# Optimization experiments

Hardware: AMD Instinct MI355X
Metric: run time of the kernel (lower is better)

## Reference

```python
import jax, jax.numpy as jnp
import numpy as np

B, H, L, D = 1, 8, 2048, 64
DP = 3   # positional coord dim
RE = 1   # extra relative features appended via concat
F = DP + RE  # LazyLinear in-features


def setup_inputs() -> dict:
    key = jax.random.key(0)
    ks = jax.random.split(key, 12)
    return {
        "q": jax.random.normal(ks[0], (B, H, L, D), jnp.float32),
        "k": jax.random.normal(ks[1], (B, H, L, D), jnp.float32),
        "v": jax.random.normal(ks[2], (B, H, L, D), jnp.float32),
        "c": jax.random.uniform(ks[3], (B, 1, 1, L), jnp.float32),
        "d_q": jax.random.normal(ks[4], (B, L, DP), jnp.float32),
        "d_k_top": jax.random.normal(ks[5], (B, L, DP), jnp.float32),
        "d_k_bot": jax.random.normal(ks[6], (B, L, DP), jnp.float32),
        "d_k_score": jax.random.uniform(ks[7], (B, L, 2, F), jnp.float32),
        "relative_top": jax.random.normal(ks[8], (B, L, L, RE), jnp.float32),
        "relative_bottom": jax.random.normal(ks[9], (B, L, L, RE), jnp.float32),
        "W_w": jax.random.normal(ks[10], (F, H), jnp.float32) * 0.1,
        "W_b": jax.random.normal(ks[11], (F, H), jnp.float32) * 0.1,
    }


def _pairwise_diff(a, b):
    # a: [B,Lq,Dp], b: [B,Lk,Dp] -> [B,Lq,Lk,Dp]
    return a[:, :, None, :] - b[:, None, :, :]


def reference(q, k, v, c, d_q, d_k_top, d_k_bot, d_k_score,
              relative_top, relative_bottom, W_w, W_b):
    # score function: scaled dot product -> [B,H,Lq,Lk]
    scores = jnp.einsum('bhqd,bhkd->bhqk', q, k) * (q.shape[-1] ** -0.5)

    # relative-position bias path
    dt = jnp.concatenate([_pairwise_diff(d_q, d_k_top), relative_top], axis=-1)     # [B,Lq,Lk,F]
    db = jnp.concatenate([_pairwise_diff(d_q, d_k_bot), relative_bottom], axis=-1)  # [B,Lq,Lk,F]
    dm = jnp.stack([dt, db], axis=3)                 # [B,Lq,Lk,2,F]
    dm = dm * d_k_score[:, None]                     # broadcast over Lq
    dm = dm.sum(axis=3)                              # [B,Lq,Lk,F]

    w = jax.nn.softplus(dm @ W_w).transpose(0, 3, 1, 2)  # [B,H,Lq,Lk]
    b = (dm @ W_b).transpose(0, 3, 1, 2)                 # [B,H,Lq,Lk]
    scores = scores * w + b

    # leaky probability function: softmax gated by per-key sampling weights c
    probs = jax.nn.softmax(scores, axis=-1) * c      # [B,H,Lq,Lk]

    out = jnp.einsum('bhqk,bhkd->bhqd', probs, v)
    return out, probs
```

## Files before the change

### kernel.cpp

```cpp
#include <hip/hip_runtime.h>
#include <cstdint>
#include <cstddef>

#define NH 8
#define LQ 2048
#define DH 64
#define NKT_Q 8

typedef __attribute__((ext_vector_type(8))) __bf16 bf16x8;
typedef __attribute__((ext_vector_type(8))) unsigned short ushort8;
typedef __attribute__((ext_vector_type(4))) float floatx4;

__device__ __forceinline__ unsigned short bf_trunc(float x) {
    return (unsigned short)(__float_as_uint(x) >> 16);
}
__device__ __forceinline__ float bf_up(unsigned short h) {
    return __uint_as_float(((unsigned int)h) << 16);
}
__device__ __forceinline__ unsigned short bf_rne(float x) {
    unsigned int u = __float_as_uint(x);
    return (unsigned short)((u + 0x7FFFu + ((u >> 16) & 1u)) >> 16);
}
struct hl_t { unsigned short h, l; };
__device__ __forceinline__ hl_t split2(float x) {
    hl_t r;
    r.h = bf_trunc(x);
    r.l = bf_trunc(x - bf_up(r.h));
    return r;
}

#define MFMA16(A, B, C) __builtin_amdgcn_mfma_f32_16x16x32_bf16((A), (B), (C), 0, 0, 0)

template <bool FAST>
__global__ __launch_bounds__(256, 3) void attn_main(
    const float* __restrict__ qp,  const float* __restrict__ kp,
    const float* __restrict__ vp,  const float* __restrict__ cp,
    const float* __restrict__ dqp, const float* __restrict__ dktp,
    const float* __restrict__ dkbp,const float* __restrict__ dksp,
    const float* __restrict__ rtp, const float* __restrict__ rbp,
    const float* __restrict__ Wwp, const float* __restrict__ Wbp,
    float* __restrict__ probp, float* __restrict__ lws, float* __restrict__ pvws,
    unsigned short* __restrict__ ews)
{
    __shared__ unsigned short sh_khi[64 * 72];
    __shared__ unsigned short sh_klo[64 * 72];
    __shared__ unsigned short sh_vhi[64 * 72];
    __shared__ unsigned short sh_vlo[64 * 72];
    __shared__ float sh_meta[64 * 13];
    __shared__ float sh_dqs[64 * 3];

    const int bid  = blockIdx.x;
    const int quar = bid & 3;
    const int h    = (bid >> 2) & 7;
    const int qt   = bid >> 5;
    const int q0   = qt * 64;
    const int t    = threadIdx.x;
    const int lane = t & 63;
    const int m    = lane & 15;
    const int quad = lane >> 4;
    const int w16  = (t >> 6) * 16;

    float Ww[4], Wb[4];
#pragma unroll
    for (int f = 0; f < 4; ++f) { Ww[f] = Wwp[f * NH + h]; Wb[f] = Wbp[f * NH + h]; }

    {
        const int row = t >> 2, s = t & 3;
        const float* src = qp + ((size_t)(h * LQ + q0 + row)) * DH + s * 16;
        ushort8 vh0, vh1, vl0, vl1;
#pragma unroll
        for (int j = 0; j < 2; ++j) {
            float4 x = *(const float4*)(src + 4 * j);
            hl_t a = split2(x.x * 0.125f), b = split2(x.y * 0.125f);
            hl_t c = split2(x.z * 0.125f), d = split2(x.w * 0.125f);
            vh0[4 * j + 0] = a.h; vl0[4 * j + 0] = a.l;
            vh0[4 * j + 1] = b.h; vl0[4 * j + 1] = b.l;
            vh0[4 * j + 2] = c.h; vl0[4 * j + 2] = c.l;
            vh0[4 * j + 3] = d.h; vl0[4 * j + 3] = d.l;
        }
#pragma unroll
        for (int j = 0; j < 2; ++j) {
            float4 x = *(const float4*)(src + 8 + 4 * j);
            hl_t a = split2(x.x * 0.125f), b = split2(x.y * 0.125f);
            hl_t c = split2(x.z * 0.125f), d = split2(x.w * 0.125f);
            vh1[4 * j + 0] = a.h; vl1[4 * j + 0] = a.l;
            vh1[4 * j + 1] = b.h; vl1[4 * j + 1] = b.l;
            vh1[4 * j + 2] = c.h; vl1[4 * j + 2] = c.l;
            vh1[4 * j + 3] = d.h; vl1[4 * j + 3] = d.l;
        }
        const int base = row * 72 + s * 16;
        *(ushort8*)&sh_khi[base] = vh0;  *(ushort8*)&sh_khi[base + 8] = vh1;
        *(ushort8*)&sh_klo[base] = vl0;  *(ushort8*)&sh_klo[base + 8] = vl1;
        if (t < 64) {
            sh_dqs[t * 3 + 0] = dqp[(q0 + t) * 3 + 0];
            sh_dqs[t * 3 + 1] = dqp[(q0 + t) * 3 + 1];
            sh_dqs[t * 3 + 2] = dqp[(q0 + t) * 3 + 2];
        }
    }
    __syncthreads();

    bf16x8 aqh[2], aql[2];
#pragma unroll
    for (int kc = 0; kc < 2; ++kc) {
        aqh[kc] = *(const bf16x8*)&sh_khi[(w16 + m) * 72 + kc * 32 + quad * 8];
        aql[kc] = *(const bf16x8*)&sh_klo[(w16 + m) * 72 + kc * 32 + quad * 8];
    }
    float dq0[4], dq1[4], dq2[4];
#pragma unroll
    for (int r = 0; r < 4; ++r) {
        const int row = w16 + quad * 4 + r;
        dq0[r] = sh_dqs[row * 3 + 0]; dq1[r] = sh_dqs[row * 3 + 1]; dq2[r] = sh_dqs[row * 3 + 2];
    }
    __syncthreads();

    const floatx4 zf = {0.f, 0.f, 0.f, 0.f};
    floatx4 pacc[4] = {zf, zf, zf, zf};
    float lpart[4] = {0.f, 0.f, 0.f, 0.f};

    for (int kth = 0; kth < NKT_Q; ++kth) {
        const int k0 = (quar * NKT_Q + kth) * 64;

        {
            const int row = t >> 2, s = t & 3;
            const float* src = kp + ((size_t)(h * LQ + k0 + row)) * DH + s * 16;
            ushort8 vh0, vh1, vl0, vl1;
#pragma unroll
            for (int j = 0; j < 2; ++j) {
                float4 x = *(const float4*)(src + 4 * j);
                hl_t a = split2(x.x), b = split2(x.y), c = split2(x.z), d = split2(x.w);
                vh0[4 * j + 0] = a.h; vl0[4 * j + 0] = a.l;
                vh0[4 * j + 1] = b.h; vl0[4 * j + 1] = b.l;
                vh0[4 * j + 2] = c.h; vl0[4 * j + 2] = c.l;
                vh0[4 * j + 3] = d.h; vl0[4 * j + 3] = d.l;
            }
#pragma unroll
            for (int j = 0; j < 2; ++j) {
                float4 x = *(const float4*)(src + 8 + 4 * j);
                hl_t a = split2(x.x), b = split2(x.y), c = split2(x.z), d = split2(x.w);
                vh1[4 * j + 0] = a.h; vl1[4 * j + 0] = a.l;
                vh1[4 * j + 1] = b.h; vl1[4 * j + 1] = b.l;
                vh1[4 * j + 2] = c.h; vl1[4 * j + 2] = c.l;
                vh1[4 * j + 3] = d.h; vl1[4 * j + 3] = d.l;
            }
            const int base = row * 72 + s * 16;
            *(ushort8*)&sh_khi[base] = vh0;  *(ushort8*)&sh_khi[base + 8] = vh1;
            *(ushort8*)&sh_klo[base] = vl0;  *(ushort8*)&sh_klo[base + 8] = vl1;
        }
        {
            const int p = t >> 4;
            const int mm = t & 15;
#pragma unroll
            for (int g = 0; g < 2; ++g) {
                const int kka = 2 * p + 32 * g;
                const float ca = cp[k0 + kka], cb = cp[k0 + kka + 1];
                const float* va = vp + ((size_t)(h * LQ + k0 + kka)) * DH;
                const float* vb = va + DH;
#pragma unroll
                for (int dd = 0; dd < 4; ++dd) {
                    const int d = mm + 16 * dd;
                    hl_t xa = split2(va[d] * ca);
                    hl_t xb = split2(vb[d] * cb);
                    *(unsigned int*)&sh_vhi[d * 72 + kka] = (unsigned int)xa.h | ((unsigned int)xb.h << 16);
                    *(unsigned int*)&sh_vlo[d * 72 + kka] = (unsigned int)xa.l | ((unsigned int)xb.l << 16);
                }
            }
        }
        if (t < 64) {
            const int kg = k0 + t;
            const float* sc_ = dksp + (size_t)kg * 8;
            const float* tp  = dktp + (size_t)kg * 3;
            const float* bt  = dkbp + (size_t)kg * 3;
            float cw = 0.f, cb2 = 0.f;
#pragma unroll
            for (int f = 0; f < 3; ++f) {
                const float stf = sc_[f], sbf = sc_[4 + f];
                const float A  = stf + sbf;
                const float Bv = tp[f] * stf + bt[f] * sbf;
                sh_meta[t * 13 + f]     = A * Ww[f];
                sh_meta[t * 13 + 4 + f] = A * Wb[f];
                cw  -= Bv * Ww[f];
                cb2 -= Bv * Wb[f];
            }
            sh_meta[t * 13 + 3]  = cw;              sh_meta[t * 13 + 7]  = cb2;
            sh_meta[t * 13 + 8]  = sc_[3] * Ww[3];  sh_meta[t * 13 + 9]  = sc_[7] * Ww[3];
            sh_meta[t * 13 + 10] = sc_[3] * Wb[3];  sh_meta[t * 13 + 11] = sc_[7] * Wb[3];
        }
        __syncthreads();

        float rt_[4][4], rb_[4][4];
#pragma unroll
        for (int r = 0; r < 4; ++r) {
            const size_t q = (size_t)(q0 + w16 + quad * 4 + r);
#pragma unroll
            for (int nt = 0; nt < 4; ++nt) {
                rt_[nt][r] = rtp[q * LQ + k0 + nt * 16 + m];
                rb_[nt][r] = rbp[q * LQ + k0 + nt * 16 + m];
            }
        }

        floatx4 sc[4] = {zf, zf, zf, zf};
#pragma unroll
        for (int nt = 0; nt < 4; ++nt) {
#pragma unroll
            for (int kc = 0; kc < 2; ++kc) {
                const int kb = (nt * 16 + m) * 72 + kc * 32 + quad * 8;
                bf16x8 bh = *(const bf16x8*)&sh_khi[kb];
                bf16x8 bl = *(const bf16x8*)&sh_klo[kb];
                sc[nt] = MFMA16(aqh[kc], bh, sc[nt]);
                sc[nt] = MFMA16(aql[kc], bh, sc[nt]);
                sc[nt] = MFMA16(aqh[kc], bl, sc[nt]);
            }
        }
        __syncthreads();

        unsigned short* ebf = sh_klo;
#pragma unroll
        for (int nt = 0; nt < 4; ++nt) {
            const int kcol = nt * 16 + m;
            const float m0 = sh_meta[kcol * 13 + 0],  m1 = sh_meta[kcol * 13 + 1];
            const float m2 = sh_meta[kcol * 13 + 2],  m3 = sh_meta[kcol * 13 + 3];
            const float m4 = sh_meta[kcol * 13 + 4],  m5 = sh_meta[kcol * 13 + 5];
            const float m6 = sh_meta[kcol * 13 + 6],  m7 = sh_meta[kcol * 13 + 7];
            const float m8 = sh_meta[kcol * 13 + 8],  m9 = sh_meta[kcol * 13 + 9];
            const float mA = sh_meta[kcol * 13 + 10], mB = sh_meta[kcol * 13 + 11];
#pragma unroll
            for (int r = 0; r < 4; ++r) {
                float ww = fmaf(dq0[r], m0, m3); ww = fmaf(dq1[r], m1, ww); ww = fmaf(dq2[r], m2, ww);
                ww = fmaf(rt_[nt][r], m8, ww);   ww = fmaf(rb_[nt][r], m9, ww);
                float bb = fmaf(dq0[r], m4, m7); bb = fmaf(dq1[r], m5, bb); bb = fmaf(dq2[r], m6, bb);
                bb = fmaf(rt_[nt][r], mA, bb);   bb = fmaf(rb_[nt][r], mB, bb);
                const float wg = __logf(1.0f + __builtin_amdgcn_exp2f(ww * 1.44269504f));
                const float sv = fmaf(sc[nt][r], wg, bb);
                const float e  = __builtin_amdgcn_exp2f(fmaf(sv, 1.44269504f, -11.5415603f));
                lpart[r] += e;
                if (!FAST)
                    probp[((size_t)(h * LQ + q0 + w16 + quad * 4 + r)) * LQ + k0 + kcol] = e;
                ebf[(w16 + quad * 4 + r) * 72 + kcol] = bf_rne(e);
            }
        }

        bf16x8 ap0 = *(const bf16x8*)&ebf[(w16 + m) * 72 + quad * 8];
        bf16x8 ap1 = *(const bf16x8*)&ebf[(w16 + m) * 72 + 32 + quad * 8];
#pragma unroll
        for (int nt = 0; nt < 4; ++nt) {
            const int vb = (nt * 16 + m) * 72 + quad * 8;
            bf16x8 bh0 = *(const bf16x8*)&sh_vhi[vb];
            bf16x8 bl0 = *(const bf16x8*)&sh_vlo[vb];
            bf16x8 bh1 = *(const bf16x8*)&sh_vhi[vb + 32];
            bf16x8 bl1 = *(const bf16x8*)&sh_vlo[vb + 32];
            pacc[nt] = MFMA16(ap0, bh0, pacc[nt]);
            pacc[nt] = MFMA16(ap0, bl0, pacc[nt]);
            pacc[nt] = MFMA16(ap1, bh1, pacc[nt]);
            pacc[nt] = MFMA16(ap1, bl1, pacc[nt]);
        }

        if (FAST) {
            const int rrow = w16 + (lane >> 2);
#pragma unroll
            for (int it = 0; it < 2; ++it) {
                const int cc = (lane & 3) + it * 4;
                ushort8 v = *(const ushort8*)&ebf[rrow * 72 + cc * 8];
                *(ushort8*)(ews + ((size_t)(h * LQ + q0 + rrow)) * LQ + k0 + cc * 8) = v;
            }
        }
        __syncthreads();
    }

#pragma unroll
    for (int off = 1; off < 16; off <<= 1) {
#pragma unroll
        for (int r = 0; r < 4; ++r) lpart[r] += __shfl_xor(lpart[r], off, 64);
    }
    if (m == 0) {
#pragma unroll
        for (int r = 0; r < 4; ++r)
            lws[quar * (NH * LQ) + h * LQ + q0 + w16 + quad * 4 + r] = lpart[r];
    }
#pragma unroll
    for (int nt = 0; nt < 4; ++nt) {
#pragma unroll
        for (int r = 0; r < 4; ++r) {
            const size_t row = (size_t)(h * LQ + q0 + w16 + quad * 4 + r);
            pvws[(size_t)quar * (NH * LQ * DH) + row * DH + nt * 16 + m] = pacc[nt][r];
        }
    }
}

__global__ void combine_kernel(const float* __restrict__ pvws, const float* __restrict__ lws,
                               float* __restrict__ outp)
{
    const int idx4 = blockIdx.x * 256 + threadIdx.x;
    const int row  = idx4 >> 4;
    const int d4   = (idx4 & 15) * 4;
    const size_t stride = (size_t)NH * LQ * DH;
    floatx4 s = {0.f, 0.f, 0.f, 0.f};
    float l = 0.f;
#pragma unroll
    for (int qr = 0; qr < 4; ++qr) {
        s += *(const floatx4*)(pvws + qr * stride + (size_t)row * DH + d4);
        l += lws[qr * (NH * LQ) + row];
    }
    const float rl = 1.0f / l;
    *(floatx4*)(outp + (size_t)row * DH + d4) = s * rl;
}

__global__ __launch_bounds__(256) void finalize_kernel(const unsigned short* __restrict__ ews,
                                                       const float* __restrict__ cp,
                                                       const float* __restrict__ lws,
                                                       float* __restrict__ probp)
{
    const int gid = blockIdx.x * 256 + threadIdx.x;
    const int row = gid >> 8;
    const int k   = (gid & 255) * 8;
    float l = 0.f;
#pragma unroll
    for (int qr = 0; qr < 4; ++qr) l += lws[qr * (NH * LQ) + row];
    const float rl = 1.0f / l;
    const ushort8 e = *(const ushort8*)(ews + (size_t)row * LQ + k);
    const floatx4 c0 = *(const floatx4*)(cp + k);
    const floatx4 c1 = *(const floatx4*)(cp + k + 4);
    floatx4 o0, o1;
#pragma unroll
    for (int j = 0; j < 4; ++j) o0[j] = bf_up(e[j]) * c0[j] * rl;
#pragma unroll
    for (int j = 0; j < 4; ++j) o1[j] = bf_up(e[4 + j]) * c1[j] * rl;
    __builtin_nontemporal_store(o0, (floatx4*)(probp + (size_t)row * LQ + k));
    __builtin_nontemporal_store(o1, (floatx4*)(probp + (size_t)row * LQ + k + 4));
}

__global__ __launch_bounds__(256) void norm_kernel(float* __restrict__ probp,
                                                   const float* __restrict__ cp,
                                                   const float* __restrict__ lws)
{
    const int r0 = blockIdx.x * 4;
    const int t  = threadIdx.x;
    const floatx4 c0 = *(const floatx4*)(cp + t * 4);
    const floatx4 c1 = *(const floatx4*)(cp + (t + 256) * 4);
#pragma unroll
    for (int r = 0; r < 4; ++r) {
        const int row = r0 + r;
        float l = 0.f;
#pragma unroll
        for (int qr = 0; qr < 4; ++qr) l += lws[qr * (NH * LQ) + row];
        const float rl = 1.0f / l;
        float* p = probp + (size_t)row * LQ;
        floatx4 x0 = *(const floatx4*)(p + t * 4);
        floatx4 x1 = *(const floatx4*)(p + (t + 256) * 4);
        x0 = x0 * c0 * rl;
        x1 = x1 * c1 * rl;
        __builtin_nontemporal_store(x0, (floatx4*)(p + t * 4));
        __builtin_nontemporal_store(x1, (floatx4*)(p + (t + 256) * 4));
    }
}

extern "C" void kernel_launch(void* const* d_in, const int* in_sizes, int n_in,
                              void* d_out, int out_size, void* d_ws, size_t ws_size,
                              hipStream_t stream)
{
    (void)in_sizes; (void)n_in; (void)out_size;
    const float* qp   = (const float*)d_in[0];
    const float* kp   = (const float*)d_in[1];
    const float* vp   = (const float*)d_in[2];
    const float* cp   = (const float*)d_in[3];
    const float* dqp  = (const float*)d_in[4];
    const float* dktp = (const float*)d_in[5];
    const float* dkbp = (const float*)d_in[6];
    const float* dksp = (const float*)d_in[7];
    const float* rtp  = (const float*)d_in[8];
    const float* rbp  = (const float*)d_in[9];
    const float* Wwp  = (const float*)d_in[10];
    const float* Wbp  = (const float*)d_in[11];

    float* outp  = (float*)d_out;
    float* probp = (float*)d_out + (size_t)NH * LQ * DH;

    float* lws  = (float*)d_ws;
    float* pvws = (float*)d_ws + 4 * (NH * LQ);
    unsigned short* ews = (unsigned short*)(pvws + (size_t)4 * NH * LQ * DH);

    const size_t need = (size_t)4 * NH * LQ * 4
                      + (size_t)4 * NH * LQ * DH * 4
                      + (size_t)NH * LQ * LQ * 2;
    const bool fast = ws_size >= need;

    if (fast) {
        attn_main<true><<<dim3(1024), dim3(256), 0, stream>>>(
            qp, kp, vp, cp, dqp, dktp, dkbp, dksp, rtp, rbp, Wwp, Wbp, probp, lws, pvws, ews);
        combine_kernel<<<dim3(1024), dim3(256), 0, stream>>>(pvws, lws, outp);
        finalize_kernel<<<dim3(16384), dim3(256), 0, stream>>>(ews, cp, lws, probp);
    } else {
        attn_main<false><<<dim3(1024), dim3(256), 0, stream>>>(
            qp, kp, vp, cp, dqp, dktp, dkbp, dksp, rtp, rbp, Wwp, Wbp, probp, lws, pvws, ews);
        combine_kernel<<<dim3(1024), dim3(256), 0, stream>>>(pvws, lws, outp);
        norm_kernel<<<dim3(4096), dim3(256), 0, stream>>>(probp, cp, lws);
    }
}
```

Baseline: 322.2 us.

## Drop low-half bf16 split for V in PV matmul and restructure finalize indexing

V (scaled by c) is now rounded once to bf16 instead of being split into hi/lo bf16 halves, which halves the PV MFMA count, removes one shared-memory buffer and its stores and loads. Separately, the finalize kernel gives each block one row and has each thread handle two 4-wide chunks with a coalesced layout. The precision drop in the PV product risks larger output error, and the lower LDS use may allow higher occupancy.

```diff
diff --git a/kernel.cpp b/kernel.cpp
--- a/kernel.cpp
+++ b/kernel.cpp
@@ -9,6 +9,7 @@
 
 typedef __attribute__((ext_vector_type(8))) __bf16 bf16x8;
 typedef __attribute__((ext_vector_type(8))) unsigned short ushort8;
+typedef __attribute__((ext_vector_type(4))) unsigned short ushort4v;
 typedef __attribute__((ext_vector_type(4))) float floatx4;
 
 __device__ __forceinline__ unsigned short bf_trunc(float x) {
@@ -45,7 +46,6 @@
     __shared__ unsigned short sh_khi[64 * 72];
     __shared__ unsigned short sh_klo[64 * 72];
     __shared__ unsigned short sh_vhi[64 * 72];
-    __shared__ unsigned short sh_vlo[64 * 72];
     __shared__ float sh_meta[64 * 13];
     __shared__ float sh_dqs[64 * 3];
 
@@ -158,10 +158,9 @@
 #pragma unroll
                 for (int dd = 0; dd < 4; ++dd) {
                     const int d = mm + 16 * dd;
-                    hl_t xa = split2(va[d] * ca);
-                    hl_t xb = split2(vb[d] * cb);
-                    *(unsigned int*)&sh_vhi[d * 72 + kka] = (unsigned int)xa.h | ((unsigned int)xb.h << 16);
-                    *(unsigned int*)&sh_vlo[d * 72 + kka] = (unsigned int)xa.l | ((unsigned int)xb.l << 16);
+                    const unsigned short ha = bf_rne(va[d] * ca);
+                    const unsigned short hb = bf_rne(vb[d] * cb);
+                    *(unsigned int*)&sh_vhi[d * 72 + kka] = (unsigned int)ha | ((unsigned int)hb << 16);
                 }
             }
         }
@@ -245,13 +244,9 @@
         for (int nt = 0; nt < 4; ++nt) {
             const int vb = (nt * 16 + m) * 72 + quad * 8;
             bf16x8 bh0 = *(const bf16x8*)&sh_vhi[vb];
-            bf16x8 bl0 = *(const bf16x8*)&sh_vlo[vb];
             bf16x8 bh1 = *(const bf16x8*)&sh_vhi[vb + 32];
-            bf16x8 bl1 = *(const bf16x8*)&sh_vlo[vb + 32];
             pacc[nt] = MFMA16(ap0, bh0, pacc[nt]);
-            pacc[nt] = MFMA16(ap0, bl0, pacc[nt]);
             pacc[nt] = MFMA16(ap1, bh1, pacc[nt]);
-            pacc[nt] = MFMA16(ap1, bl1, pacc[nt]);
         }
 
         if (FAST) {
@@ -309,23 +304,24 @@
                                                        const float* __restrict__ lws,
                                                        float* __restrict__ probp)
 {
-    const int gid = blockIdx.x * 256 + threadIdx.x;
-    const int row = gid >> 8;
-    const int k   = (gid & 255) * 8;
+    const int row = blockIdx.x;
+    const int t   = threadIdx.x;
     float l = 0.f;
 #pragma unroll
     for (int qr = 0; qr < 4; ++qr) l += lws[qr * (NH * LQ) + row];
     const float rl = 1.0f / l;
-    const ushort8 e = *(const ushort8*)(ews + (size_t)row * LQ + k);
-    const floatx4 c0 = *(const floatx4*)(cp + k);
-    const floatx4 c1 = *(const floatx4*)(cp + k + 4);
-    floatx4 o0, o1;
-#pragma unroll
-    for (int j = 0; j < 4; ++j) o0[j] = bf_up(e[j]) * c0[j] * rl;
-#pragma unroll
-    for (int j = 0; j < 4; ++j) o1[j] = bf_up(e[4 + j]) * c1[j] * rl;
-    __builtin_nontemporal_store(o0, (floatx4*)(probp + (size_t)row * LQ + k));
-    __builtin_nontemporal_store(o1, (floatx4*)(probp + (size_t)row * LQ + k + 4));
+
+    const size_t base = (size_t)row * LQ;
+#pragma unroll
+    for (int g = 0; g < 2; ++g) {
+        const int k = g * 1024 + t * 4;
+        const ushort4v e = *(const ushort4v*)(ews + base + k);
+        const floatx4 c = *(const floatx4*)(cp + k);
+        floatx4 o;
+#pragma unroll
+        for (int j = 0; j < 4; ++j) o[j] = bf_up(e[j]) * c[j] * rl;
+        __builtin_nontemporal_store(o, (floatx4*)(probp + base + k));
+    }
 }
 
 __global__ __launch_bounds__(256) void norm_kernel(float* __restrict__ probp,
```

Measured after the change: 307.2 us. -4.7%, faster.
